# Optimization experiments

Hardware: AMD Instinct MI355X
Metric: run time of the kernel (lower is better)

Reference implementation:

```python
import jax, jax.numpy as jnp
import numpy as np

L, H, E, V, BS = 12, 12, 768, 50257, 1024  # layers, heads, n_embd, vocab, block_size
B, T = 2, 1024
D = E // H


def setup_inputs() -> dict:
    key = jax.random.key(0)
    ks = jax.random.split(key, 10)
    s = 0.02
    d = {}
    d["idx"] = jax.random.randint(ks[0], (B, T), 0, V)
    d["targets"] = jax.random.randint(ks[1], (B, T), 0, V)
    # embeddings (wte tied with lm_head)
    d["wte"] = (jax.random.normal(ks[2], (V, E)) * s).astype(jnp.float32)
    d["wpe"] = (jax.random.normal(ks[3], (BS, E)) * s).astype(jnp.float32)
    # stacked per-layer params; Linear weights stored [in, out] (= torch W.T)
    d["ln1_w"] = jnp.ones((L, E), jnp.float32)
    d["ln1_b"] = jnp.zeros((L, E), jnp.float32)
    d["attn_w"] = (jax.random.normal(ks[4], (L, E, 3 * E)) * s).astype(jnp.float32)
    d["attn_b"] = jnp.zeros((L, 3 * E), jnp.float32)
    d["proj_w"] = (jax.random.normal(ks[5], (L, E, E)) * s).astype(jnp.float32)
    d["proj_b"] = jnp.zeros((L, E), jnp.float32)
    d["ln2_w"] = jnp.ones((L, E), jnp.float32)
    d["ln2_b"] = jnp.zeros((L, E), jnp.float32)
    d["fc_w"] = (jax.random.normal(ks[6], (L, E, 4 * E)) * s).astype(jnp.float32)
    d["fc_b"] = jnp.zeros((L, 4 * E), jnp.float32)
    d["fcproj_w"] = (jax.random.normal(ks[7], (L, 4 * E, E)) * s).astype(jnp.float32)
    d["fcproj_b"] = jnp.zeros((L, E), jnp.float32)
    d["lnf_w"] = jnp.ones((E,), jnp.float32)
    d["lnf_b"] = jnp.zeros((E,), jnp.float32)
    return d


def _ln(x, w, b, eps=1e-5):
    m = jnp.mean(x, -1, keepdims=True)
    v = jnp.mean(jnp.square(x - m), -1, keepdims=True)
    return (x - m) * jax.lax.rsqrt(v + eps) * w + b


def _block(x, p, mask):
    l1w, l1b, aw, ab, pw, pb, l2w, l2b, fw, fb, fpw, fpb = p
    Bx, Tx, C = x.shape
    # causal self-attention (explicit QK^T + mask + softmax + AV, as in source)
    qkv = _ln(x, l1w, l1b) @ aw + ab                       # [B,T,3E]
    q, k, v = jnp.split(qkv, 3, axis=-1)
    q = q.reshape(Bx, Tx, H, D).transpose(0, 2, 1, 3)       # [B,H,T,D]
    k = k.reshape(Bx, Tx, H, D).transpose(0, 2, 1, 3)
    v = v.reshape(Bx, Tx, H, D).transpose(0, 2, 1, 3)
    att = jnp.einsum('bhqd,bhkd->bhqk', q, k) * (1.0 / np.sqrt(D))
    att = jnp.where(mask, att, -jnp.inf)
    att = jax.nn.softmax(att, axis=-1)
    y = jnp.einsum('bhqk,bhkd->bhqd', att, v)
    y = y.transpose(0, 2, 1, 3).reshape(Bx, Tx, C)
    x = x + y @ pw + pb
    # MLP with tanh-approx GELU
    h = jax.nn.gelu(_ln(x, l2w, l2b) @ fw + fb, approximate=True)
    x = x + h @ fpw + fpb
    return x


def reference(idx, targets, wte, wpe, ln1_w, ln1_b, attn_w, attn_b, proj_w, proj_b,
              ln2_w, ln2_b, fc_w, fc_b, fcproj_w, fcproj_b, lnf_w, lnf_b):
    Tq = idx.shape[1]
    x = wte[idx] + wpe[:Tq]                                 # [B,T,E]
    mask = jnp.tril(jnp.ones((Tq, Tq), dtype=bool))

    def step(x, p):
        return _block(x, p, mask), None

    layer_params = (ln1_w, ln1_b, attn_w, attn_b, proj_w, proj_b,
                    ln2_w, ln2_b, fc_w, fc_b, fcproj_w, fcproj_b)
    x, _ = jax.lax.scan(step, x, layer_params)
    x = _ln(x, lnf_w, lnf_b)
    logits = x @ wte.T                                      # tied lm_head, [B,T,V]
    logp = jax.nn.log_softmax(logits, axis=-1)
    nll = -jnp.take_along_axis(logp, targets[..., None], axis=-1)[..., 0]
    loss = jnp.mean(nll)
    return logits, loss
```

## Files before the change

kernel.cpp:

```cpp
#include <hip/hip_runtime.h>
#include <hip/hip_bf16.h>
#include <math.h>

#define LNUM 12
#define HNUM 12
#define EDIM 768
#define VDIM 50257
#define BDIM 2
#define TDIM 1024
#define BT (BDIM*TDIM)
#define E3 (3*EDIM)
#define E4 (4*EDIM)
#define NPB (2*((VDIM+127)/128))

typedef __bf16 bf16x8 __attribute__((ext_vector_type(8)));
typedef __bf16 bf16x4 __attribute__((ext_vector_type(4)));
typedef float f32x4 __attribute__((ext_vector_type(4)));

__device__ __forceinline__ float gelu_f(float x) {
    float u = 0.7978845608028654f * (x + 0.044715f * x * x * x);
    return 0.5f * x * (1.0f + tanhf(u));
}

__device__ __forceinline__ void gl16(const void* g, void* l) {
    __builtin_amdgcn_global_load_lds(
        (const __attribute__((address_space(1))) unsigned int*)g,
        (__attribute__((address_space(3))) unsigned int*)l,
        16, 0, 0);
}

__global__ __launch_bounds__(256) void embed_kernel(
    const int* __restrict__ idx, const float* __restrict__ wte,
    const float* __restrict__ wpe, float* __restrict__ x)
{
    const int row = blockIdx.x;
    const int t = row % TDIM;
    const int tok = idx[row];
    const float* we = wte + (size_t)tok * EDIM;
    const float* pe = wpe + (size_t)t * EDIM;
    float* xr = x + (size_t)row * EDIM;
    for (int e = threadIdx.x; e < EDIM; e += 256) xr[e] = we[e] + pe[e];
}

__global__ __launch_bounds__(256) void ln_kernel(
    const float* __restrict__ in, const float* __restrict__ w,
    const float* __restrict__ b, __bf16* __restrict__ out)
{
    const int row = blockIdx.x * 4 + (threadIdx.x >> 6);
    const int lane = threadIdx.x & 63;
    const float4* xr = (const float4*)(in + (size_t)row * EDIM);
    float4 a0 = xr[lane], a1 = xr[64 + lane], a2 = xr[128 + lane];
    float s = a0.x + a0.y + a0.z + a0.w + a1.x + a1.y + a1.z + a1.w
            + a2.x + a2.y + a2.z + a2.w;
    #pragma unroll
    for (int off = 32; off; off >>= 1) s += __shfl_xor(s, off);
    const float mean = s * (1.0f / EDIM);
    float4 d0 = make_float4(a0.x - mean, a0.y - mean, a0.z - mean, a0.w - mean);
    float4 d1 = make_float4(a1.x - mean, a1.y - mean, a1.z - mean, a1.w - mean);
    float4 d2 = make_float4(a2.x - mean, a2.y - mean, a2.z - mean, a2.w - mean);
    float v = d0.x*d0.x + d0.y*d0.y + d0.z*d0.z + d0.w*d0.w
            + d1.x*d1.x + d1.y*d1.y + d1.z*d1.z + d1.w*d1.w
            + d2.x*d2.x + d2.y*d2.y + d2.z*d2.z + d2.w*d2.w;
    #pragma unroll
    for (int off = 32; off; off >>= 1) v += __shfl_xor(v, off);
    const float inv = rsqrtf(v * (1.0f / EDIM) + 1e-5f);
    const float4* w4 = (const float4*)w;
    const float4* b4 = (const float4*)b;
    __bf16* orow = out + (size_t)row * EDIM;
    #pragma unroll
    for (int c = 0; c < 3; ++c) {
        float4 dd = c == 0 ? d0 : (c == 1 ? d1 : d2);
        float4 ww = w4[c * 64 + lane], bb = b4[c * 64 + lane];
        bf16x4 o;
        o[0] = (__bf16)(dd.x * inv * ww.x + bb.x);
        o[1] = (__bf16)(dd.y * inv * ww.y + bb.y);
        o[2] = (__bf16)(dd.z * inv * ww.z + bb.z);
        o[3] = (__bf16)(dd.w * inv * ww.w + bb.w);
        *(bf16x4*)(orow + c * 256 + lane * 4) = o;
    }
}

__global__ __launch_bounds__(256) void redln_kernel(
    const float* __restrict__ ps, const float* __restrict__ bias,
    float* __restrict__ x, const float* __restrict__ w,
    const float* __restrict__ b, __bf16* __restrict__ out)
{
    const int row = blockIdx.x * 4 + (threadIdx.x >> 6);
    const int lane = threadIdx.x & 63;
    const float4* p0 = (const float4*)(ps + (size_t)row * EDIM);
    const float4* p1 = (const float4*)(ps + (size_t)(BT + row) * EDIM);
    float4* xr = (float4*)(x + (size_t)row * EDIM);
    const float4* b4 = (const float4*)bias;
    float4 a[3];
    #pragma unroll
    for (int c = 0; c < 3; ++c) {
        const int i = c * 64 + lane;
        float4 u = p0[i], v = p1[i], xx = xr[i], bb = b4[i];
        a[c] = make_float4(u.x + v.x + xx.x + bb.x, u.y + v.y + xx.y + bb.y,
                           u.z + v.z + xx.z + bb.z, u.w + v.w + xx.w + bb.w);
        xr[i] = a[c];
    }
    float s = a[0].x + a[0].y + a[0].z + a[0].w + a[1].x + a[1].y + a[1].z + a[1].w
            + a[2].x + a[2].y + a[2].z + a[2].w;
    #pragma unroll
    for (int off = 32; off; off >>= 1) s += __shfl_xor(s, off);
    const float mean = s * (1.0f / EDIM);
    float v = 0.f;
    #pragma unroll
    for (int c = 0; c < 3; ++c) {
        a[c] = make_float4(a[c].x - mean, a[c].y - mean, a[c].z - mean, a[c].w - mean);
        v += a[c].x * a[c].x + a[c].y * a[c].y + a[c].z * a[c].z + a[c].w * a[c].w;
    }
    #pragma unroll
    for (int off = 32; off; off >>= 1) v += __shfl_xor(v, off);
    const float inv = rsqrtf(v * (1.0f / EDIM) + 1e-5f);
    const float4* w4 = (const float4*)w;
    const float4* lb4 = (const float4*)b;
    __bf16* orow = out + (size_t)row * EDIM;
    #pragma unroll
    for (int c = 0; c < 3; ++c) {
        float4 ww = w4[c * 64 + lane], bb = lb4[c * 64 + lane];
        bf16x4 o;
        o[0] = (__bf16)(a[c].x * inv * ww.x + bb.x);
        o[1] = (__bf16)(a[c].y * inv * ww.y + bb.y);
        o[2] = (__bf16)(a[c].z * inv * ww.z + bb.z);
        o[3] = (__bf16)(a[c].w * inv * ww.w + bb.w);
        *(bf16x4*)(orow + c * 256 + lane * 4) = o;
    }
}

__global__ __launch_bounds__(256) void convt_kernel(
    const float* __restrict__ in, __bf16* __restrict__ out, int K, int N)
{
    in  += (size_t)blockIdx.z * K * N;
    out += (size_t)blockIdx.z * K * N;
    __shared__ float t[32][33];
    const int n0 = blockIdx.x * 32, k0 = blockIdx.y * 32;
    const int r = threadIdx.x >> 3, c = (threadIdx.x & 7) * 4;
    float4 v = *(const float4*)(in + (size_t)(k0 + r) * N + n0 + c);
    t[r][c + 0] = v.x; t[r][c + 1] = v.y; t[r][c + 2] = v.z; t[r][c + 3] = v.w;
    __syncthreads();
    bf16x4 o;
    o[0] = (__bf16)t[c + 0][r];
    o[1] = (__bf16)t[c + 1][r];
    o[2] = (__bf16)t[c + 2][r];
    o[3] = (__bf16)t[c + 3][r];
    *(bf16x4*)(out + (size_t)(n0 + r) * K + k0 + c) = o;
}

__global__ __launch_bounds__(256) void cvt_kernel(
    const float* __restrict__ in, __bf16* __restrict__ out, long n4)
{
    for (long i = blockIdx.x * 256L + threadIdx.x; i < n4; i += (long)gridDim.x * 256L) {
        float4 v = ((const float4*)in)[i];
        out[i * 4 + 0] = (__bf16)v.x;
        out[i * 4 + 1] = (__bf16)v.y;
        out[i * 4 + 2] = (__bf16)v.z;
        out[i * 4 + 3] = (__bf16)v.w;
    }
}

template<int BM, int BN, int BK, bool BIAS, bool GELU_, bool RES_, bool OUTBF, bool NGUARD, bool LOGITS>
__global__ __launch_bounds__(256, 2) void mgemm(
    const __bf16* __restrict__ A, const __bf16* __restrict__ Bt,
    const float* __restrict__ bias, const float* __restrict__ res,
    void* __restrict__ Cout, float* __restrict__ part, int M, int N, int K, int lda)
{
    constexpr int WM = BM / 2, WN = BN / 2;
    constexpr int FM = WM / 16, FN = WN / 16;
    constexpr int KS = BK / 32;
    constexpr int TBA = BM * BK * 2;
    constexpr int TBB = BN * BK * 2;
    constexpr int rA = TBA / 4096, rB = TBB / 4096;
    constexpr int RPI = 2048 / BK;
    constexpr int CPR = BK / 8;
    __shared__ __align__(16) __bf16 As[3 * BM * BK];
    __shared__ __align__(16) __bf16 Bs[3 * BN * BK];
    const int tid = threadIdx.x;
    const int lane = tid & 63;
    const int wave = tid >> 6;
    const int wr = wave >> 1, wc = wave & 1;

    int bm, bn;
    if (LOGITS) {
        const int wg = blockIdx.x;
        bm = (wg >> 3) & 7;
        bn = (wg & 7) + ((wg >> 6) << 3);
        if (bn * BN >= N) return;
    } else { bm = blockIdx.y; bn = blockIdx.x; }
    const int m0 = bm * BM;
    const int n0 = bn * BN;
    const int kbase = blockIdx.z * K;
    const size_t zoff = (size_t)blockIdx.z * M * N;

    const int srow = tid / CPR;
    const int skey = (BK == 32) ? ((srow >> 1) & 3) : (srow & 7);
    const int c0 = (tid % CPR) ^ skey;

    const __bf16* gA = A + (size_t)(m0 + srow) * lda + kbase + c0 * 8;
    const __bf16* gB[rB];
    #pragma unroll
    for (int r = 0; r < rB; ++r) {
        int nr = n0 + srow + r * RPI;
        if (NGUARD) nr = nr < N ? nr : N - 1;
        gB[r] = Bt + (size_t)nr * lda + kbase + c0 * 8;
    }

    const int fr = lane & 15;
    const int g = lane >> 4;
    const int fkey = (BK == 32) ? ((fr >> 1) & 3) : (fr & 7);

    f32x4 acc[FM][FN];
    #pragma unroll
    for (int i = 0; i < FM; i++)
        #pragma unroll
        for (int j = 0; j < FN; j++) acc[i][j] = (f32x4){0.f, 0.f, 0.f, 0.f};

    const int nt = K / BK;

    auto stage = [&](int kk, int b) {
        #pragma unroll
        for (int r = 0; r < rA; ++r)
            gl16(gA + (size_t)r * RPI * lda + kk, (char*)As + b * TBA + r * 4096 + tid * 16);
        #pragma unroll
        for (int r = 0; r < rB; ++r)
            gl16(gB[r] + kk, (char*)Bs + b * TBB + r * 4096 + tid * 16);
    };

    stage(0, 0);
    if (nt > 1) stage(BK, 1);

    int b0 = 0, b1 = 1, b2 = 2;
    for (int t = 0; t < nt; ++t) {
        if (t + 1 < nt) {
            static_assert(rA + rB == 4 || rA + rB == 6, "vmcnt literal");
            if constexpr (rA + rB == 4) asm volatile("s_waitcnt vmcnt(4)" ::: "memory");
            else                        asm volatile("s_waitcnt vmcnt(6)" ::: "memory");
        } else {
            asm volatile("s_waitcnt vmcnt(0)" ::: "memory");
        }
        asm volatile("s_barrier" ::: "memory");
        if (t + 2 < nt) stage((t + 2) * BK, b2);

        const char* pa = (const char*)As + b0 * TBA;
        const char* pb = (const char*)Bs + b0 * TBB;
        bf16x8 af[FM][KS], bfr[FN][KS];
        #pragma unroll
        for (int i = 0; i < FM; i++)
            #pragma unroll
            for (int kc = 0; kc < KS; kc++)
                af[i][kc] = *(const bf16x8*)(pa + (wr * WM + i * 16 + fr) * (2 * BK)
                                                + (((kc * 4 + g) ^ fkey) << 4));
        #pragma unroll
        for (int j = 0; j < FN; j++)
            #pragma unroll
            for (int kc = 0; kc < KS; kc++)
                bfr[j][kc] = *(const bf16x8*)(pb + (wc * WN + j * 16 + fr) * (2 * BK)
                                                 + (((kc * 4 + g) ^ fkey) << 4));
        #pragma unroll
        for (int kc = 0; kc < KS; kc++)
            #pragma unroll
            for (int i = 0; i < FM; i++)
                #pragma unroll
                for (int j = 0; j < FN; j++)
                    acc[i][j] = __builtin_amdgcn_mfma_f32_16x16x32_bf16(af[i][kc], bfr[j][kc], acc[i][j], 0, 0, 0);
        const int tmp = b0; b0 = b1; b1 = b2; b2 = tmp;
    }

    const int crow = g * 4;
    if constexpr (LOGITS) {
        constexpr int NH = WN / 64;
        const int cg0 = bn * (BN / 64) + wc * NH;
        #pragma unroll
        for (int i = 0; i < FM; i++) {
            #pragma unroll
            for (int r = 0; r < 4; r++) {
                const int m = m0 + wr * WM + i * 16 + crow + r;
                float se[NH];
                #pragma unroll
                for (int h = 0; h < NH; h++) se[h] = 0.f;
                #pragma unroll
                for (int j = 0; j < FN; j++) {
                    const int n = n0 + wc * WN + j * 16 + fr;
                    if (n < N) {
                        float v = acc[i][j][r];
                        ((float*)Cout)[(size_t)m * N + n] = v;
                        se[j >> 2] += __expf(v);
                    }
                }
                #pragma unroll
                for (int h = 0; h < NH; h++) {
                    float sh = se[h];
                    sh += __shfl_xor(sh, 1); sh += __shfl_xor(sh, 2);
                    sh += __shfl_xor(sh, 4); sh += __shfl_xor(sh, 8);
                    if (fr == 0 && (n0 + wc * WN + h * 64) < N)
                        part[(size_t)m * NPB + cg0 + h] = sh;
                }
            }
        }
    } else {
        #pragma unroll
        for (int i = 0; i < FM; i++) {
            #pragma unroll
            for (int r = 0; r < 4; r++) {
                const int m = m0 + wr * WM + i * 16 + crow + r;
                #pragma unroll
                for (int j = 0; j < FN; j++) {
                    const int n = n0 + wc * WN + j * 16 + fr;
                    if (!NGUARD || n < N) {
                        float v = acc[i][j][r];
                        if (BIAS) v += bias[n];
                        if (GELU_) v = gelu_f(v);
                        if (RES_) v += res[(size_t)m * N + n];
                        if (OUTBF) ((__bf16*)Cout)[zoff + (size_t)m * N + n] = (__bf16)v;
                        else       ((float*)Cout)[zoff + (size_t)m * N + n] = v;
                    }
                }
            }
        }
    }
}

__global__ __launch_bounds__(128) void fattn_kernel(
    const __bf16* __restrict__ qkv, __bf16* __restrict__ y)
{
    const int bq = gridDim.x - 1 - blockIdx.x;
    const int h = blockIdx.y, b = blockIdx.z;
    const int tid = threadIdx.x, lane = tid & 63, w = tid >> 6;
    const int fr = lane & 15, g = lane >> 4;

    __shared__ __align__(16) __bf16 Ks[64 * 64];
    __shared__ __align__(16) __bf16 Vt[64 * 64];
    __shared__ __align__(16) __bf16 Ps[2][16 * 64];

    const __bf16* base = qkv + (size_t)b * TDIM * E3;
    const int q0w = bq * 32 + w * 16;
    const int NT = (bq >> 1) + 1;
    const int last = NT - 1;

    bf16x8 qf[2];
    {
        const __bf16* qp = base + (size_t)(q0w + fr) * E3 + h * 64 + g * 8;
        qf[0] = *(const bf16x8*)qp;
        qf[1] = *(const bf16x8*)(qp + 32);
    }

    const int r0 = tid >> 3, ch = tid & 7;
    bf16x8 kr[4], vr[4];

    #pragma unroll
    for (int it = 0; it < 4; ++it) {
        const int row = it * 16 + r0;
        const __bf16* gp = base + (size_t)row * E3 + EDIM + h * 64 + ch * 8;
        kr[it] = *(const bf16x8*)gp;
        vr[it] = *(const bf16x8*)(gp + EDIM);
    }
    #pragma unroll
    for (int it = 0; it < 4; ++it) {
        const int row = it * 16 + r0;
        *(bf16x8*)(Ks + row * 64 + ((ch ^ (row & 7)) << 3)) = kr[it];
        #pragma unroll
        for (int j = 0; j < 8; ++j) {
            const int d = ch * 8 + j;
            const int key = ((d >> 3) ^ d) & 7;
            Vt[d * 64 + ((((row >> 3) ^ key) << 3) + (row & 7))] = vr[it][j];
        }
    }
    __syncthreads();

    float m[4] = {-1e30f, -1e30f, -1e30f, -1e30f};
    float l[4] = {0.f, 0.f, 0.f, 0.f};
    f32x4 acc[4];
    #pragma unroll
    for (int jd = 0; jd < 4; ++jd) acc[jd] = (f32x4){0.f, 0.f, 0.f, 0.f};

    for (int kt = 0; kt < NT; ++kt) {
        if (kt < last) {
            const int k1 = (kt + 1) * 64;
            #pragma unroll
            for (int it = 0; it < 4; ++it) {
                const int row = it * 16 + r0;
                const __bf16* gp = base + (size_t)(k1 + row) * E3 + EDIM + h * 64 + ch * 8;
                kr[it] = *(const bf16x8*)gp;
                vr[it] = *(const bf16x8*)(gp + EDIM);
            }
        }

        const int k0 = kt * 64;
        f32x4 s[4];
        __builtin_amdgcn_s_setprio(1);
        #pragma unroll
        for (int jf = 0; jf < 4; ++jf) {
            const int krow = jf * 16 + fr;
            f32x4 sv = (f32x4){0.f, 0.f, 0.f, 0.f};
            #pragma unroll
            for (int kc = 0; kc < 2; ++kc) {
                bf16x8 kf = *(const bf16x8*)(Ks + krow * 64 + (((kc * 4 + g) ^ (fr & 7)) << 3));
                sv = __builtin_amdgcn_mfma_f32_16x16x32_bf16(qf[kc], kf, sv, 0, 0, 0);
            }
            s[jf] = sv;
        }
        __builtin_amdgcn_s_setprio(0);
        #pragma unroll
        for (int jf = 0; jf < 4; ++jf)
            #pragma unroll
            for (int r = 0; r < 4; ++r) s[jf][r] *= 0.125f;
        if (kt == last) {
            #pragma unroll
            for (int jf = 0; jf < 4; ++jf) {
                const int k = k0 + jf * 16 + fr;
                #pragma unroll
                for (int r = 0; r < 4; ++r) {
                    const int q = q0w + g * 4 + r;
                    if (k > q) s[jf][r] = -1e30f;
                }
            }
        }

        #pragma unroll
        for (int r = 0; r < 4; ++r) {
            float mx = fmaxf(fmaxf(s[0][r], s[1][r]), fmaxf(s[2][r], s[3][r]));
            mx = fmaxf(mx, __shfl_xor(mx, 1));
            mx = fmaxf(mx, __shfl_xor(mx, 2));
            mx = fmaxf(mx, __shfl_xor(mx, 4));
            mx = fmaxf(mx, __shfl_xor(mx, 8));
            const float mn = fmaxf(m[r], mx);
            const float sc2 = __expf(m[r] - mn);
            m[r] = mn;
            float rs = 0.f;
            #pragma unroll
            for (int jf = 0; jf < 4; ++jf) {
                const float p = __expf(s[jf][r] - mn);
                s[jf][r] = p;
                rs += p;
            }
            rs += __shfl_xor(rs, 1);
            rs += __shfl_xor(rs, 2);
            rs += __shfl_xor(rs, 4);
            rs += __shfl_xor(rs, 8);
            l[r] = l[r] * sc2 + rs;
            #pragma unroll
            for (int jd = 0; jd < 4; ++jd) acc[jd][r] *= sc2;
        }

        __bf16* pw = &Ps[w][0];
        #pragma unroll
        for (int jf = 0; jf < 4; ++jf) {
            const int chp = jf * 2 + (fr >> 3);
            #pragma unroll
            for (int r = 0; r < 4; ++r) {
                const int row = g * 4 + r;
                pw[row * 64 + (((chp ^ (row & 7)) << 3) + (fr & 7))] = (__bf16)s[jf][r];
            }
        }
        asm volatile("s_waitcnt lgkmcnt(0)" ::: "memory");
        bf16x8 pa[2];
        #pragma unroll
        for (int kc = 0; kc < 2; ++kc)
            pa[kc] = *(const bf16x8*)(pw + fr * 64 + (((kc * 4 + g) ^ (fr & 7)) << 3));

        __builtin_amdgcn_s_setprio(1);
        #pragma unroll
        for (int jd = 0; jd < 4; ++jd) {
            const int d = jd * 16 + fr;
            const int key = ((d >> 3) ^ d) & 7;
            #pragma unroll
            for (int kc = 0; kc < 2; ++kc) {
                bf16x8 vf = *(const bf16x8*)(Vt + d * 64 + (((kc * 4 + g) ^ key) << 3));
                acc[jd] = __builtin_amdgcn_mfma_f32_16x16x32_bf16(pa[kc], vf, acc[jd], 0, 0, 0);
            }
        }
        __builtin_amdgcn_s_setprio(0);

        if (kt < last) {
            __syncthreads();
            #pragma unroll
            for (int it = 0; it < 4; ++it) {
                const int row = it * 16 + r0;
                *(bf16x8*)(Ks + row * 64 + ((ch ^ (row & 7)) << 3)) = kr[it];
                #pragma unroll
                for (int j = 0; j < 8; ++j) {
                    const int d = ch * 8 + j;
                    const int key = ((d >> 3) ^ d) & 7;
                    Vt[d * 64 + ((((row >> 3) ^ key) << 3) + (row & 7))] = vr[it][j];
                }
            }
            __syncthreads();
        }
    }

    #pragma unroll
    for (int r = 0; r < 4; ++r) {
        const float inv = 1.0f / l[r];
        const int q = q0w + g * 4 + r;
        __bf16* yp = y + ((size_t)(b * TDIM + q)) * EDIM + h * 64;
        #pragma unroll
        for (int jd = 0; jd < 4; ++jd)
            yp[jd * 16 + fr] = (__bf16)(acc[jd][r] * inv);
    }
}

__global__ __launch_bounds__(256) void lsefin_kernel(
    const float* __restrict__ part, const float* __restrict__ logits,
    const int* __restrict__ targets, float* __restrict__ rr)
{
    const int row = blockIdx.x, tid = threadIdx.x;
    float s = 0.f;
    for (int j = tid; j < NPB; j += 256) s += part[(size_t)row * NPB + j];
    #pragma unroll
    for (int off = 32; off; off >>= 1) s += __shfl_xor(s, off);
    __shared__ float red[4];
    if ((tid & 63) == 0) red[tid >> 6] = s;
    __syncthreads();
    if (tid == 0) {
        float S = red[0] + red[1] + red[2] + red[3];
        rr[row] = logf(S) - logits[(size_t)row * VDIM + targets[row]];
    }
}

__global__ __launch_bounds__(256) void loss_reduce_kernel(
    const float* __restrict__ rr, float* __restrict__ out)
{
    const int tid = threadIdx.x;
    float s = 0.f;
    for (int i = tid; i < BT; i += 256) s += rr[i];
    #pragma unroll
    for (int off = 32; off; off >>= 1) s += __shfl_xor(s, off);
    __shared__ float red[4];
    if ((tid & 63) == 0) red[tid >> 6] = s;
    __syncthreads();
    if (tid == 0) out[0] = (red[0] + red[1] + red[2] + red[3]) * (1.0f / BT);
}

extern "C" void kernel_launch(void* const* d_in, const int* in_sizes, int n_in,
                              void* d_out, int out_size, void* d_ws, size_t ws_size,
                              hipStream_t stream)
{
    const int*   idx     = (const int*)d_in[0];
    const int*   targets = (const int*)d_in[1];
    const float* wte     = (const float*)d_in[2];
    const float* wpe     = (const float*)d_in[3];
    const float* ln1_w   = (const float*)d_in[4];
    const float* ln1_b   = (const float*)d_in[5];
    const float* attn_w  = (const float*)d_in[6];
    const float* attn_b  = (const float*)d_in[7];
    const float* proj_w  = (const float*)d_in[8];
    const float* proj_b  = (const float*)d_in[9];
    const float* ln2_w   = (const float*)d_in[10];
    const float* ln2_b   = (const float*)d_in[11];
    const float* fc_w    = (const float*)d_in[12];
    const float* fc_b    = (const float*)d_in[13];
    const float* fcp_w   = (const float*)d_in[14];
    const float* fcp_b   = (const float*)d_in[15];
    const float* lnf_w   = (const float*)d_in[16];
    const float* lnf_b   = (const float*)d_in[17];

    float* logits = (float*)d_out;

    const size_t slq = (size_t)EDIM * E3, slp = (size_t)EDIM * EDIM;
    const size_t slf = (size_t)EDIM * E4, slfp = (size_t)E4 * EDIM;

    char* wp = (char*)d_ws;
    float*  x     = (float*)wp;   wp += (size_t)BT * EDIM * 4;
    __bf16* qkvb  = (__bf16*)wp;  wp += (size_t)BT * E3 * 2;
    __bf16* xnbf  = (__bf16*)wp;  wp += (size_t)BT * EDIM * 2;
    __bf16* ybf   = (__bf16*)wp;  wp += (size_t)BT * EDIM * 2;
    __bf16* hbf   = (__bf16*)wp;  wp += (size_t)BT * E4 * 2;
    __bf16* wteb  = (__bf16*)wp;  wp += (size_t)VDIM * EDIM * 2;
    float*  part  = (float*)wp;   wp += (size_t)BT * NPB * 4;
    float*  psum  = (float*)wp;   wp += (size_t)2 * BT * EDIM * 4;
    float*  rr    = (float*)wp;   wp += (size_t)BT * 4;
    __bf16* wqkvb = (__bf16*)wp;

    const size_t wbytes_all = (slq + slp + slf + slfp) * 2 * LNUM;
    const size_t used = (size_t)(wp - (char*)d_ws);
    const bool big = ws_size >= used + wbytes_all;
    const size_t L = big ? LNUM : 1;
    __bf16* wprjb = wqkvb + slq * L;
    __bf16* wfcb  = wprjb + slp * L;
    __bf16* wfpb  = wfcb  + slf * L;

    embed_kernel<<<BT, 256, 0, stream>>>(idx, wte, wpe, x);
    cvt_kernel<<<2048, 256, 0, stream>>>(wte, wteb, (long)VDIM * EDIM / 4);

    if (big) {
        convt_kernel<<<dim3(E3 / 32, EDIM / 32, LNUM), 256, 0, stream>>>(attn_w, wqkvb, EDIM, E3);
        convt_kernel<<<dim3(EDIM / 32, EDIM / 32, LNUM), 256, 0, stream>>>(proj_w, wprjb, EDIM, EDIM);
        convt_kernel<<<dim3(E4 / 32, EDIM / 32, LNUM), 256, 0, stream>>>(fc_w, wfcb, EDIM, E4);
        convt_kernel<<<dim3(EDIM / 32, E4 / 32, LNUM), 256, 0, stream>>>(fcp_w, wfpb, E4, EDIM);
    }

    ln_kernel<<<BT / 4, 256, 0, stream>>>(x, ln1_w, ln1_b, xnbf);

    for (int l = 0; l < LNUM; ++l) {
        const __bf16* wq = wqkvb + (big ? (size_t)l * slq : 0);
        const __bf16* wpj = wprjb + (big ? (size_t)l * slp : 0);
        const __bf16* wf = wfcb + (big ? (size_t)l * slf : 0);
        const __bf16* wfp = wfpb + (big ? (size_t)l * slfp : 0);

        if (!big)
            convt_kernel<<<dim3(E3 / 32, EDIM / 32), 256, 0, stream>>>(
                attn_w + (size_t)l * slq, (__bf16*)wq, EDIM, E3);
        mgemm<64, 64, 64, true, false, false, true, false, false>
            <<<dim3(E3 / 64, BT / 64), 256, 0, stream>>>(
            xnbf, wq, attn_b + (size_t)l * E3, nullptr, qkvb, nullptr, BT, E3, EDIM, EDIM);
        fattn_kernel<<<dim3(TDIM / 32, HNUM, BDIM), 128, 0, stream>>>(qkvb, ybf);
        if (!big)
            convt_kernel<<<dim3(EDIM / 32, EDIM / 32), 256, 0, stream>>>(
                proj_w + (size_t)l * slp, (__bf16*)wpj, EDIM, EDIM);
        mgemm<64, 64, 64, false, false, false, false, false, false>
            <<<dim3(EDIM / 64, BT / 64, 2), 256, 0, stream>>>(
            ybf, wpj, nullptr, nullptr, psum, nullptr, BT, EDIM, EDIM / 2, EDIM);
        redln_kernel<<<BT / 4, 256, 0, stream>>>(
            psum, proj_b + (size_t)l * EDIM, x,
            ln2_w + (size_t)l * EDIM, ln2_b + (size_t)l * EDIM, xnbf);
        if (!big)
            convt_kernel<<<dim3(E4 / 32, EDIM / 32), 256, 0, stream>>>(
                fc_w + (size_t)l * slf, (__bf16*)wf, EDIM, E4);
        mgemm<64, 64, 64, true, true, false, true, false, false>
            <<<dim3(E4 / 64, BT / 64), 256, 0, stream>>>(
            xnbf, wf, fc_b + (size_t)l * E4, nullptr, hbf, nullptr, BT, E4, EDIM, EDIM);
        if (!big)
            convt_kernel<<<dim3(EDIM / 32, E4 / 32), 256, 0, stream>>>(
                fcp_w + (size_t)l * slfp, (__bf16*)wfp, E4, EDIM);
        mgemm<64, 64, 64, false, false, false, false, false, false>
            <<<dim3(EDIM / 64, BT / 64, 2), 256, 0, stream>>>(
            hbf, wfp, nullptr, nullptr, psum, nullptr, BT, EDIM, E4 / 2, E4);
        const float* nw = (l + 1 < LNUM) ? ln1_w + (size_t)(l + 1) * EDIM : lnf_w;
        const float* nb = (l + 1 < LNUM) ? ln1_b + (size_t)(l + 1) * EDIM : lnf_b;
        redln_kernel<<<BT / 4, 256, 0, stream>>>(
            psum, fcp_b + (size_t)l * EDIM, x, nw, nb, xnbf);
    }

    mgemm<256, 128, 32, false, false, false, false, true, true>
        <<<dim3(64 * 50), 256, 0, stream>>>(
        xnbf, wteb, nullptr, nullptr, logits, part, BT, VDIM, EDIM, EDIM);
    lsefin_kernel<<<BT, 256, 0, stream>>>(part, logits, targets, rr);
    loss_reduce_kernel<<<1, 256, 0, stream>>>(rr, logits + (size_t)BT * VDIM);
}
```

Measured before the change: 2.016 ms.

## Add dedicated 512-thread logits GEMM with interleaved staging and MFMA priority

Replaces the templated LOGITS path of mgemm with a dedicated lgemm kernel for the tied lm_head GEMM. It uses 8 waves per 256x128 tile with BK=64 and triple-buffered LDS. Global-to-LDS staging for tile t+2 is split into halves interleaved between two MFMA phases, and s_setprio raises wave priority around the MFMA bursts. The goal is better latency hiding and MFMA utilisation on the largest GEMM. The cost is higher LDS use (144KB) and one workgroup per CU.

```diff
diff --git a/kernel.cpp b/kernel.cpp
--- a/kernel.cpp
+++ b/kernel.cpp
@@ -160,11 +160,11 @@
     }
 }
 
-template<int BM, int BN, int BK, bool BIAS, bool GELU_, bool RES_, bool OUTBF, bool NGUARD, bool LOGITS>
+template<int BM, int BN, int BK, bool BIAS, bool GELU_, bool RES_, bool OUTBF, bool NGUARD>
 __global__ __launch_bounds__(256, 2) void mgemm(
     const __bf16* __restrict__ A, const __bf16* __restrict__ Bt,
     const float* __restrict__ bias, const float* __restrict__ res,
-    void* __restrict__ Cout, float* __restrict__ part, int M, int N, int K, int lda)
+    void* __restrict__ Cout, int M, int N, int K, int lda)
 {
     constexpr int WM = BM / 2, WN = BN / 2;
     constexpr int FM = WM / 16, FN = WN / 16;
@@ -181,13 +181,7 @@
     const int wave = tid >> 6;
     const int wr = wave >> 1, wc = wave & 1;
 
-    int bm, bn;
-    if (LOGITS) {
-        const int wg = blockIdx.x;
-        bm = (wg >> 3) & 7;
-        bn = (wg & 7) + ((wg >> 6) << 3);
-        if (bn * BN >= N) return;
-    } else { bm = blockIdx.y; bn = blockIdx.x; }
+    const int bm = blockIdx.y, bn = blockIdx.x;
     const int m0 = bm * BM;
     const int n0 = bn * BN;
     const int kbase = blockIdx.z * K;
@@ -268,55 +262,157 @@
     }
 
     const int crow = g * 4;
-    if constexpr (LOGITS) {
-        constexpr int NH = WN / 64;
-        const int cg0 = bn * (BN / 64) + wc * NH;
-        #pragma unroll
-        for (int i = 0; i < FM; i++) {
-            #pragma unroll
-            for (int r = 0; r < 4; r++) {
-                const int m = m0 + wr * WM + i * 16 + crow + r;
-                float se[NH];
+    #pragma unroll
+    for (int i = 0; i < FM; i++) {
+        #pragma unroll
+        for (int r = 0; r < 4; r++) {
+            const int m = m0 + wr * WM + i * 16 + crow + r;
+            #pragma unroll
+            for (int j = 0; j < FN; j++) {
+                const int n = n0 + wc * WN + j * 16 + fr;
+                if (!NGUARD || n < N) {
+                    float v = acc[i][j][r];
+                    if (BIAS) v += bias[n];
+                    if (GELU_) v = gelu_f(v);
+                    if (RES_) v += res[(size_t)m * N + n];
+                    if (OUTBF) ((__bf16*)Cout)[zoff + (size_t)m * N + n] = (__bf16)v;
+                    else       ((float*)Cout)[zoff + (size_t)m * N + n] = v;
+                }
+            }
+        }
+    }
+}
+
+__global__ __launch_bounds__(512, 1) void lgemm(
+    const __bf16* __restrict__ A, const __bf16* __restrict__ Bt,
+    float* __restrict__ Cout, float* __restrict__ part, int M, int N, int K)
+{
+    __shared__ __align__(16) __bf16 As[3 * 256 * 64];
+    __shared__ __align__(16) __bf16 Bs[3 * 128 * 64];
+    const int tid = threadIdx.x;
+    const int lane = tid & 63;
+    const int wave = tid >> 6;
+    const int wm = wave >> 1, wn = wave & 1;
+
+    const int wg = blockIdx.x;
+    const int bm = (wg >> 3) & 7;
+    const int bn = (wg & 7) + ((wg >> 6) << 3);
+    if (bn * 128 >= N) return;
+    const int m0 = bm * 256, n0 = bn * 128;
+
+    const int srow = tid >> 3;
+    const int c0 = (tid & 7) ^ (srow & 7);
+    const __bf16* gA = A + (size_t)(m0 + srow) * K + c0 * 8;
+    const __bf16* gB[2];
+    #pragma unroll
+    for (int r = 0; r < 2; ++r) {
+        int nr = n0 + r * 64 + srow;
+        nr = nr < N ? nr : N - 1;
+        gB[r] = Bt + (size_t)nr * K + c0 * 8;
+    }
+
+    const int fr = lane & 15;
+    const int g = lane >> 4;
+    const int fk = fr & 7;
+
+    auto stageA = [&](int kk, int b, int r) {
+        gl16(gA + (size_t)r * 64 * K + kk, (char*)As + b * 32768 + r * 8192 + tid * 16);
+    };
+    auto stageB = [&](int kk, int b, int r) {
+        gl16(gB[r] + kk, (char*)Bs + b * 16384 + r * 8192 + tid * 16);
+    };
+
+    f32x4 acc[4][4];
+    #pragma unroll
+    for (int i = 0; i < 4; i++)
+        #pragma unroll
+        for (int j = 0; j < 4; j++) acc[i][j] = (f32x4){0.f, 0.f, 0.f, 0.f};
+
+    const int nt = K >> 6;
+    #pragma unroll
+    for (int r = 0; r < 4; ++r) stageA(0, 0, r);
+    #pragma unroll
+    for (int r = 0; r < 2; ++r) stageB(0, 0, r);
+    #pragma unroll
+    for (int r = 0; r < 4; ++r) stageA(64, 1, r);
+    #pragma unroll
+    for (int r = 0; r < 2; ++r) stageB(64, 1, r);
+
+    for (int t = 0; t < nt; ++t) {
+        const int bt = t % 3;
+        if (t + 1 < nt) asm volatile("s_waitcnt vmcnt(6)" ::: "memory");
+        else            asm volatile("s_waitcnt vmcnt(0)" ::: "memory");
+        asm volatile("s_barrier" ::: "memory");
+
+        const char* pa = (const char*)As + bt * 32768;
+        const char* pb = (const char*)Bs + bt * 16384;
+        const int kk2 = (t + 2) * 64;
+        const int b2 = (t + 2) % 3;
+
+        bf16x8 bfr[4][2], af[2][2];
+        #pragma unroll
+        for (int j = 0; j < 4; ++j)
+            #pragma unroll
+            for (int kc = 0; kc < 2; ++kc)
+                bfr[j][kc] = *(const bf16x8*)(pb + (wn * 64 + j * 16 + fr) * 128
+                                                 + (((kc * 4 + g) ^ fk) << 4));
+        #pragma unroll
+        for (int i = 0; i < 2; ++i)
+            #pragma unroll
+            for (int kc = 0; kc < 2; ++kc)
+                af[i][kc] = *(const bf16x8*)(pa + (wm * 64 + i * 16 + fr) * 128
+                                                + (((kc * 4 + g) ^ fk) << 4));
+        if (t + 2 < nt) { stageA(kk2, b2, 0); stageA(kk2, b2, 1); stageA(kk2, b2, 2); }
+        __builtin_amdgcn_s_setprio(1);
+        #pragma unroll
+        for (int kc = 0; kc < 2; ++kc)
+            #pragma unroll
+            for (int i = 0; i < 2; ++i)
                 #pragma unroll
-                for (int h = 0; h < NH; h++) se[h] = 0.f;
+                for (int j = 0; j < 4; ++j)
+                    acc[i][j] = __builtin_amdgcn_mfma_f32_16x16x32_bf16(af[i][kc], bfr[j][kc], acc[i][j], 0, 0, 0);
+        __builtin_amdgcn_s_setprio(0);
+
+        bf16x8 af1[2][2];
+        #pragma unroll
+        for (int i = 0; i < 2; ++i)
+            #pragma unroll
+            for (int kc = 0; kc < 2; ++kc)
+                af1[i][kc] = *(const bf16x8*)(pa + (wm * 64 + (i + 2) * 16 + fr) * 128
+                                                 + (((kc * 4 + g) ^ fk) << 4));
+        if (t + 2 < nt) { stageA(kk2, b2, 3); stageB(kk2, b2, 0); stageB(kk2, b2, 1); }
+        __builtin_amdgcn_s_setprio(1);
+        #pragma unroll
+        for (int kc = 0; kc < 2; ++kc)
+            #pragma unroll
+            for (int i = 0; i < 2; ++i)
                 #pragma unroll
-                for (int j = 0; j < FN; j++) {
-                    const int n = n0 + wc * WN + j * 16 + fr;
-                    if (n < N) {
-                        float v = acc[i][j][r];
-                        ((float*)Cout)[(size_t)m * N + n] = v;
-                        se[j >> 2] += __expf(v);
-                    }
+                for (int j = 0; j < 4; ++j)
+                    acc[i + 2][j] = __builtin_amdgcn_mfma_f32_16x16x32_bf16(af1[i][kc], bfr[j][kc], acc[i + 2][j], 0, 0, 0);
+        __builtin_amdgcn_s_setprio(0);
+    }
+
+    const int crow = g * 4;
+    const int cg = bn * 2 + wn;
+    #pragma unroll
+    for (int i = 0; i < 4; i++) {
+        #pragma unroll
+        for (int r = 0; r < 4; r++) {
+            const int m = m0 + wm * 64 + i * 16 + crow + r;
+            float se = 0.f;
+            #pragma unroll
+            for (int j = 0; j < 4; j++) {
+                const int n = n0 + wn * 64 + j * 16 + fr;
+                if (n < N) {
+                    float v = acc[i][j][r];
+                    Cout[(size_t)m * N + n] = v;
+                    se += __expf(v);
                 }
-                #pragma unroll
-                for (int h = 0; h < NH; h++) {
-                    float sh = se[h];
-                    sh += __shfl_xor(sh, 1); sh += __shfl_xor(sh, 2);
-                    sh += __shfl_xor(sh, 4); sh += __shfl_xor(sh, 8);
-                    if (fr == 0 && (n0 + wc * WN + h * 64) < N)
-                        part[(size_t)m * NPB + cg0 + h] = sh;
-                }
-            }
-        }
-    } else {
-        #pragma unroll
-        for (int i = 0; i < FM; i++) {
-            #pragma unroll
-            for (int r = 0; r < 4; r++) {
-                const int m = m0 + wr * WM + i * 16 + crow + r;
-                #pragma unroll
-                for (int j = 0; j < FN; j++) {
-                    const int n = n0 + wc * WN + j * 16 + fr;
-                    if (!NGUARD || n < N) {
-                        float v = acc[i][j][r];
-                        if (BIAS) v += bias[n];
-                        if (GELU_) v = gelu_f(v);
-                        if (RES_) v += res[(size_t)m * N + n];
-                        if (OUTBF) ((__bf16*)Cout)[zoff + (size_t)m * N + n] = (__bf16)v;
-                        else       ((float*)Cout)[zoff + (size_t)m * N + n] = v;
-                    }
-                }
-            }
+            }
+            se += __shfl_xor(se, 1); se += __shfl_xor(se, 2);
+            se += __shfl_xor(se, 4); se += __shfl_xor(se, 8);
+            if (fr == 0 && (n0 + wn * 64) < N)
+                part[(size_t)m * NPB + cg] = se;
         }
     }
 }
@@ -601,40 +697,39 @@
         if (!big)
             convt_kernel<<<dim3(E3 / 32, EDIM / 32), 256, 0, stream>>>(
                 attn_w + (size_t)l * slq, (__bf16*)wq, EDIM, E3);
-        mgemm<64, 64, 64, true, false, false, true, false, false>
+        mgemm<64, 64, 64, true, false, false, true, false>
             <<<dim3(E3 / 64, BT / 64), 256, 0, stream>>>(
-            xnbf, wq, attn_b + (size_t)l * E3, nullptr, qkvb, nullptr, BT, E3, EDIM, EDIM);
+            xnbf, wq, attn_b + (size_t)l * E3, nullptr, qkvb, BT, E3, EDIM, EDIM);
         fattn_kernel<<<dim3(TDIM / 32, HNUM, BDIM), 128, 0, stream>>>(qkvb, ybf);
         if (!big)
             convt_kernel<<<dim3(EDIM / 32, EDIM / 32), 256, 0, stream>>>(
                 proj_w + (size_t)l * slp, (__bf16*)wpj, EDIM, EDIM);
-        mgemm<64, 64, 64, false, false, false, false, false, false>
+        mgemm<64, 64, 64, false, false, false, false, false>
             <<<dim3(EDIM / 64, BT / 64, 2), 256, 0, stream>>>(
-            ybf, wpj, nullptr, nullptr, psum, nullptr, BT, EDIM, EDIM / 2, EDIM);
+            ybf, wpj, nullptr, nullptr, psum, BT, EDIM, EDIM / 2, EDIM);
         redln_kernel<<<BT / 4, 256, 0, stream>>>(
             psum, proj_b + (size_t)l * EDIM, x,
             ln2_w + (size_t)l * EDIM, ln2_b + (size_t)l * EDIM, xnbf);
         if (!big)
             convt_kernel<<<dim3(E4 / 32, EDIM / 32), 256, 0, stream>>>(
                 fc_w + (size_t)l * slf, (__bf16*)wf, EDIM, E4);
-        mgemm<64, 64, 64, true, true, false, true, false, false>
+        mgemm<64, 64, 64, true, true, false, true, false>
             <<<dim3(E4 / 64, BT / 64), 256, 0, stream>>>(
-            xnbf, wf, fc_b + (size_t)l * E4, nullptr, hbf, nullptr, BT, E4, EDIM, EDIM);
+            xnbf, wf, fc_b + (size_t)l * E4, nullptr, hbf, BT, E4, EDIM, EDIM);
         if (!big)
             convt_kernel<<<dim3(EDIM / 32, E4 / 32), 256, 0, stream>>>(
                 fcp_w + (size_t)l * slfp, (__bf16*)wfp, E4, EDIM);
-        mgemm<64, 64, 64, false, false, false, false, false, false>
+        mgemm<64, 64, 64, false, false, false, false, false>
             <<<dim3(EDIM / 64, BT / 64, 2), 256, 0, stream>>>(
-            hbf, wfp, nullptr, nullptr, psum, nullptr, BT, EDIM, E4 / 2, E4);
+            hbf, wfp, nullptr, nullptr, psum, BT, EDIM, E4 / 2, E4);
         const float* nw = (l + 1 < LNUM) ? ln1_w + (size_t)(l + 1) * EDIM : lnf_w;
         const float* nb = (l + 1 < LNUM) ? ln1_b + (size_t)(l + 1) * EDIM : lnf_b;
         redln_kernel<<<BT / 4, 256, 0, stream>>>(
             psum, fcp_b + (size_t)l * EDIM, x, nw, nb, xnbf);
     }
 
-    mgemm<256, 128, 32, false, false, false, false, true, true>
-        <<<dim3(64 * 50), 256, 0, stream>>>(
-        xnbf, wteb, nullptr, nullptr, logits, part, BT, VDIM, EDIM, EDIM);
+    lgemm<<<dim3(64 * 50), 512, 0, stream>>>(
+        xnbf, wteb, logits, part, BT, VDIM, EDIM);
     lsefin_kernel<<<BT, 256, 0, stream>>>(part, logits, targets, rr);
     loss_reduce_kernel<<<1, 256, 0, stream>>>(rr, logits + (size_t)BT * VDIM);
 }
```

New measurement: 2.022 ms. No clear change (+0.3%).
